# Kernel optimization log

Hardware: AMD Instinct MI355X
Metric: run time of the kernel (lower is better)

Reference implementation:

```python
import jax, jax.numpy as jnp
import numpy as np

N_AQI, N_MEO = 35, 18
N = N_AQI + N_MEO
F_OUT = 64
CTX = 60
D = F_OUT + CTX            # per-node feature dim inside pairwise concat
ALPHA = 0.2                # leakyrelu negative slope
B = 4096
IN_AQI, IN_MEO = 16, 16
NEG = -1e12


def _xavier(key, shape):
    fan_in, fan_out = shape[0], shape[-1]
    gain = 1.414
    bound = gain * np.sqrt(6.0 / (fan_in + fan_out))
    return jax.random.uniform(key, shape, jnp.float32, -bound, bound)


def setup_inputs() -> dict:
    key = jax.random.key(0)
    ks = jax.random.split(key, 32)
    inp = {
        "aqi_inp": jax.random.normal(ks[0], (B, N_AQI, IN_AQI), jnp.float32),
        "meo_inp": jax.random.normal(ks[1], (B, N_MEO, IN_MEO), jnp.float32),
        "context_feat": jax.random.normal(ks[2], (N, CTX), jnp.float32),
        "adj_norm": jax.random.uniform(ks[3], (N, N), jnp.float32),
        # embedding tables (all 2-dim embeddings as in the module)
        "aqi_idE": jax.random.normal(ks[4], (35, 2), jnp.float32),
        "aqi_monthE": jax.random.normal(ks[5], (13, 2), jnp.float32),
        "aqi_weekdayE": jax.random.normal(ks[6], (7, 2), jnp.float32),
        "aqi_hourE": jax.random.normal(ks[7], (24, 2), jnp.float32),
        "meo_windE": jax.random.normal(ks[8], (9, 2), jnp.float32),
        "meo_idE": jax.random.normal(ks[9], (18, 2), jnp.float32),
        "meo_monthE": jax.random.normal(ks[10], (13, 2), jnp.float32),
        "meo_weekdayE": jax.random.normal(ks[11], (7, 2), jnp.float32),
        "meo_hourE": jax.random.normal(ks[12], (24, 2), jnp.float32),
        # projection weights
        "W_xa": _xavier(ks[13], (IN_AQI, F_OUT)),
        "W_xm": _xavier(ks[14], (IN_MEO, F_OUT)),
        "W_ua": _xavier(ks[15], (IN_AQI + 8, F_OUT)),
        "W_um": _xavier(ks[16], (IN_MEO + 10, F_OUT)),
        # attention vectors: 2*F_OUT + 121 = 2*D + 1
        "a_aa": _xavier(ks[17], (2 * F_OUT + 121, 1)),
        "a_am": _xavier(ks[18], (2 * F_OUT + 121, 1)),
        "a_ma": _xavier(ks[19], (2 * F_OUT + 121, 1)),
        "a_mm": _xavier(ks[20], (2 * F_OUT + 121, 1)),
        # integer inputs
        "aqi_ex": jax.random.randint(ks[21], (B, N_AQI, 4), 0, 7, jnp.int32),
        "meo_ex": jax.random.randint(ks[22], (B, N_MEO, 5), 0, 7, jnp.int32),
        "adj": jax.random.randint(ks[23], (N, N), 0, 2, jnp.int32),
    }
    return inp


def _block(hf_src, hf_dst, an_block, a):
    # e[b,i,j] = leakyrelu(hf_src[b,i].a_src + hf_dst[b,j].a_dst + an[i,j]*a_last)
    d = hf_src.shape[-1]
    s = hf_src @ a[:d, 0]                        # [B, Ns]
    t = hf_dst @ a[d:2 * d, 0]                   # [B, Nd]
    e = s[:, :, None] + t[:, None, :] + an_block * a[2 * d, 0]
    return jax.nn.leaky_relu(e, ALPHA)


def reference(aqi_inp, meo_inp, context_feat, adj_norm,
              aqi_idE, aqi_monthE, aqi_weekdayE, aqi_hourE,
              meo_windE, meo_idE, meo_monthE, meo_weekdayE, meo_hourE,
              W_xa, W_xm, W_ua, W_um, a_aa, a_am, a_ma, a_mm,
              aqi_ex, meo_ex, adj):
    # value projection (pre-embedding features)
    attri_aqi = aqi_inp @ W_xa                   # [B, 35, F]
    attri_meo = meo_inp @ W_xm                   # [B, 18, F]
    heter_attri = jnp.concatenate([attri_aqi, attri_meo], axis=1)  # [B, 53, F]

    # append external-feature embeddings
    aqi_full = jnp.concatenate([
        aqi_inp, aqi_idE[aqi_ex[:, :, 0]], aqi_monthE[aqi_ex[:, :, 1]],
        aqi_weekdayE[aqi_ex[:, :, 2]], aqi_hourE[aqi_ex[:, :, 3]]], axis=2)
    meo_full = jnp.concatenate([
        meo_inp, meo_windE[meo_ex[:, :, 0]], meo_idE[meo_ex[:, :, 1]],
        meo_monthE[meo_ex[:, :, 2]], meo_weekdayE[meo_ex[:, :, 3]],
        meo_hourE[meo_ex[:, :, 4]]], axis=2)

    heter_aqi = aqi_full @ W_ua                  # [B, 35, F]
    heter_meo = meo_full @ W_um                  # [B, 18, F]
    hf = jnp.concatenate([heter_aqi, heter_meo], axis=1)            # [B, 53, F]
    ctx = jnp.broadcast_to(context_feat[None], (hf.shape[0], N, CTX))
    hf = jnp.concatenate([hf, ctx], axis=2)      # [B, 53, D]

    # pairwise scores per heterogeneous sub-block (decomposed, no N*N*D tensor)
    hfa, hfm = hf[:, :N_AQI], hf[:, N_AQI:]
    e_aa = _block(hfa, hfa, adj_norm[:N_AQI, :N_AQI], a_aa)
    e_am = _block(hfa, hfm, adj_norm[:N_AQI, N_AQI:], a_am)
    e_ma = _block(hfm, hfa, adj_norm[N_AQI:, :N_AQI], a_ma)
    e_mm = _block(hfm, hfm, adj_norm[N_AQI:, N_AQI:], a_mm)
    e = jnp.concatenate([
        jnp.concatenate([e_aa, e_am], axis=2),
        jnp.concatenate([e_ma, e_mm], axis=2)], axis=1)             # [B, 53, 53]

    attention = jax.nn.softmax(jnp.where(adj[None] > 0, e, NEG), axis=2)
    heter_out = attention @ heter_attri          # [B, 53, F]
    return heter_out[:, :N_AQI, :], heter_out[:, N_AQI:, :]
```

## Files before the change

kernel.cpp:

```cpp
#include <hip/hip_runtime.h>

#define NAQ 35
#define NME 18
#define NN  53
#define FD  64
#define CTXD 60
#define WAVES 8

typedef unsigned int   u32;
typedef unsigned short u16;
typedef short s8v __attribute__((ext_vector_type(8)));
typedef float f4v __attribute__((ext_vector_type(4)));

#define WS_EB_F  1280
#define WS_FLAG  4672

__device__ __forceinline__ float ldf(const void* p, long i, bool bf) {
  if (bf) { u16 h = ((const u16*)p)[i]; return __uint_as_float(((u32)h) << 16); }
  return ((const float*)p)[i];
}
__device__ __forceinline__ u16 f2bf(float f) {
  u32 u = __float_as_uint(f);
  return (u16)((u + 0x7FFFu + ((u >> 16) & 1u)) >> 16);
}
__device__ __forceinline__ float bf2f(u16 h) {
  return __uint_as_float(((u32)h) << 16);
}
__device__ __forceinline__ u32 pk2(float a, float b) {
  return (u32)f2bf(a) | ((u32)f2bf(b) << 16);
}
__device__ __forceinline__ bool sniff_bf16(const void* ctx) {
  const u32* w = (const u32*)ctx;
  bool ok = true;
#pragma unroll
  for (int k = 0; k < 32; ++k) {
    u32 e = (w[k] >> 7) & 0xFFu;
    ok = ok && (e >= 96u && e <= 160u);
  }
  return ok;
}
__device__ __forceinline__ s8v ld_fragu(const u16* p) {
  union { float4 f; s8v s; } u;
  u.f = *(const float4*)(const void*)p;
  return u.s;
}
__device__ __forceinline__ s8v pack8f(float4 a, float4 b) {
  union { u32 u[4]; s8v s; } U;
  U.u[0] = pk2(a.x, a.y);
  U.u[1] = pk2(a.z, a.w);
  U.u[2] = pk2(b.x, b.y);
  U.u[3] = pk2(b.z, b.w);
  return U.s;
}
__device__ __forceinline__ s8v load_inp8(const void* p, long idx, bool bf) {
  if (bf) {
    union { uint4 u; s8v s; } U;
    U.u = *(const uint4*)((const u16*)p + idx);
    return U.s;
  }
  float4 f0 = *(const float4*)((const float*)p + idx);
  float4 f1 = *(const float4*)((const float*)p + idx + 4);
  return pack8f(f0, f1);
}
__device__ __forceinline__ void pack_hl(const float* e, s8v* hi, s8v* lo) {
  union { u32 u[4]; s8v s; } H, L;
#pragma unroll
  for (int w = 0; w < 4; ++w) {
    u16 h0 = f2bf(e[2*w]), h1 = f2bf(e[2*w+1]);
    float l0 = e[2*w] - bf2f(h0), l1 = e[2*w+1] - bf2f(h1);
    H.u[w] = (u32)h0 | ((u32)h1 << 16);
    L.u[w] = (u32)f2bf(l0) | ((u32)f2bf(l1) << 16);
  }
  *hi = H.s; *lo = L.s;
}
__device__ __forceinline__ void avsel(int tr,
    const void* a_aa, const void* a_am, const void* a_ma, const void* a_mm,
    const void** av, int* off) {
  switch (tr) {
    case 0: *av = a_aa; *off = 0;   break;
    case 1: *av = a_am; *off = 0;   break;
    case 2: *av = a_aa; *off = 124; break;
    case 3: *av = a_ma; *off = 124; break;
    case 4: *av = a_ma; *off = 0;   break;
    case 5: *av = a_mm; *off = 0;   break;
    case 6: *av = a_am; *off = 124; break;
    default:*av = a_mm; *off = 124; break;
  }
}

__global__ void prep_kernel(
    const void* __restrict__ ctx, const void* __restrict__ adjn,
    const void* __restrict__ Wxa, const void* __restrict__ Wxm,
    const void* __restrict__ Wua, const void* __restrict__ Wum,
    const void* __restrict__ a_aa, const void* __restrict__ a_am,
    const void* __restrict__ a_ma, const void* __restrict__ a_mm,
    const int* __restrict__ adj, float* __restrict__ ws)
{
  const bool bf = sniff_bf16(ctx);
  int tid = blockIdx.x * blockDim.x + threadIdx.x;
  if (tid == 0) ws[WS_FLAG] = bf ? 1.f : 0.f;
  if (tid < 2048) {
    int n = tid >> 5, kk = tid & 31;
    float v = (kk < 16) ? ldf(Wxa, kk * 64 + n, bf)
                        : ldf(Wxm, (kk - 16) * 64 + n, bf);
    ((u16*)ws)[tid] = f2bf(v);
    return;
  }
  if (tid < 2560) {
    int idx = tid - 2048;
    int half = idx >> 8, rem = idx & 255;
    int role = rem >> 6, k = rem & 63;
    float w = 0.f;
    const void* Wu = nullptr; int kk = -1, tr = 0;
    if (k < 16)      { Wu = Wua; kk = k;           tr = role;     }
    else if (k < 32) { Wu = Wum; kk = k - 16;      tr = 4 + role; }
    else if (k < 40) { Wu = Wua; kk = 16 + (k-32); tr = role;     }
    else if (k < 50) { Wu = Wum; kk = 16 + (k-40); tr = 4 + role; }
    if (kk >= 0) {
      const void* av; int off;
      avsel(tr, a_aa, a_am, a_ma, a_mm, &av, &off);
      float s = 0.f;
      for (int f = 0; f < 64; ++f) s += ldf(Wu, kk * 64 + f, bf) * ldf(av, off + f, bf);
      w = s;
    }
    u16 hi = f2bf(w);
    u16 val = hi;
    if (half) { float lo = w - bf2f(hi); val = f2bf(lo); }
    ((u16*)ws)[2048 + idx] = val;
    return;
  }
  if (tid < 5952) {
    int e = tid - 2560;
    int r = e >> 6, j = e & 63;
    float v = 1e30f;
    if (j < NN && adj[r * NN + j] > 0) {
      const void* aq = (r < NAQ) ? ((j < NAQ) ? a_aa : a_am)
                                 : ((j < NAQ) ? a_ma : a_mm);
      float s = ldf(adjn, r * NN + j, bf) * ldf(aq, 248, bf);
      for (int c = 0; c < CTXD; ++c) {
        s += ldf(ctx, r * CTXD + c, bf) * ldf(aq, 64 + c, bf);
        s += ldf(ctx, j * CTXD + c, bf) * ldf(aq, 188 + c, bf);
      }
      v = s;
    }
    ws[WS_EB_F + e] = v;
  }
}

__global__ __launch_bounds__(512, 4) void hga_main(
    const void* __restrict__ aqi_inp, const void* __restrict__ meo_inp,
    const void* __restrict__ ctx,
    const void* __restrict__ aqi_idE, const void* __restrict__ aqi_monthE,
    const void* __restrict__ aqi_weekdayE, const void* __restrict__ aqi_hourE,
    const void* __restrict__ meo_windE, const void* __restrict__ meo_idE,
    const void* __restrict__ meo_monthE, const void* __restrict__ meo_weekdayE,
    const void* __restrict__ meo_hourE,
    const int* __restrict__ aqi_ex, const int* __restrict__ meo_ex,
    const float* __restrict__ ws, void* __restrict__ out, int B)
{
  __shared__ __align__(16) u16  sWtA[64 * 40];
  __shared__ __align__(16) u16  sWtPhi[16 * 72];
  __shared__ __align__(16) u16  sWtPlo[16 * 72];
  __shared__ __align__(16) float sEB[64 * 68];
  __shared__ __align__(16) float sSVW[WAVES * 256];

  const int t = threadIdx.x;
  const bool bf = (ws[WS_FLAG] != 0.f);
  const int wv = t >> 6, lane = t & 63;
  const int mm = lane & 15, q4 = lane >> 4;
  const int b = blockIdx.x * WAVES + wv;
  const bool valid = (b < B);

  s8v av0[4], a1h[4], a1l[4];
  const s8v zero8 = {0, 0, 0, 0, 0, 0, 0, 0};
#pragma unroll
  for (int i = 0; i < 4; ++i) { av0[i] = zero8; a1h[i] = zero8; a1l[i] = zero8; }
  if (valid) {
#pragma unroll
    for (int i = 0; i < 4; ++i) {
      const int r = 16 * i + mm;
      s8v v0 = zero8, vh = zero8, vl = zero8;
      if (r < NN) {
        if (r < NAQ) {
          if (q4 < 2) v0 = load_inp8(aqi_inp, ((long)b * NAQ + r) * 16 + q4 * 8, bf);
          if (q4 == 0) {
            const int4 ix = *(const int4*)(aqi_ex + ((long)b * NAQ + r) * 4);
            float e[8];
            e[0] = ldf(aqi_idE,      ix.x * 2, bf);  e[1] = ldf(aqi_idE,      ix.x * 2 + 1, bf);
            e[2] = ldf(aqi_monthE,   ix.y * 2, bf);  e[3] = ldf(aqi_monthE,   ix.y * 2 + 1, bf);
            e[4] = ldf(aqi_weekdayE, ix.z * 2, bf);  e[5] = ldf(aqi_weekdayE, ix.z * 2 + 1, bf);
            e[6] = ldf(aqi_hourE,    ix.w * 2, bf);  e[7] = ldf(aqi_hourE,    ix.w * 2 + 1, bf);
            pack_hl(e, &vh, &vl);
          }
        } else {
          const int ri = r - NAQ;
          if (q4 >= 2) v0 = load_inp8(meo_inp, ((long)b * NME + ri) * 16 + (q4 - 2) * 8, bf);
          if (q4 == 1) {
            const int* ix = meo_ex + ((long)b * NME + ri) * 5;
            float e[8];
            e[0] = ldf(meo_windE,    ix[0] * 2, bf); e[1] = ldf(meo_windE,    ix[0] * 2 + 1, bf);
            e[2] = ldf(meo_idE,      ix[1] * 2, bf); e[3] = ldf(meo_idE,      ix[1] * 2 + 1, bf);
            e[4] = ldf(meo_monthE,   ix[2] * 2, bf); e[5] = ldf(meo_monthE,   ix[2] * 2 + 1, bf);
            e[6] = ldf(meo_weekdayE, ix[3] * 2, bf); e[7] = ldf(meo_weekdayE, ix[3] * 2 + 1, bf);
            pack_hl(e, &vh, &vl);
          } else if (q4 == 2) {
            int i4 = meo_ex[((long)b * NME + ri) * 5 + 4];
            float e[8] = {0.f, 0.f, 0.f, 0.f, 0.f, 0.f, 0.f, 0.f};
            e[0] = ldf(meo_hourE, i4 * 2, bf);  e[1] = ldf(meo_hourE, i4 * 2 + 1, bf);
            pack_hl(e, &vh, &vl);
          }
        }
      }
      av0[i] = v0; a1h[i] = vh; a1l[i] = vl;
    }
  }

  for (int u = t; u < 256; u += 512) {
    int row = u >> 2, c = u & 3;
    *(uint4*)(sWtA + row * 40 + c * 8) = ((const uint4*)ws)[u];
  }
  for (int u = t; u < 256; u += 512) {
    int half = u >> 7, u2 = u & 127;
    int row = u2 >> 3, c = u2 & 7;
    uint4 v = make_uint4(0, 0, 0, 0);
    if (row < 4) v = ((const uint4*)ws)[256 + half * 32 + row * 8 + c];
    u16* dst = half ? sWtPlo : sWtPhi;
    *(uint4*)(dst + row * 72 + c * 8) = v;
  }
  for (int u = t; u < 1024; u += 512) {
    int r = u >> 4, f = u & 15;
    float4 v4 = make_float4(1e30f, 1e30f, 1e30f, 1e30f);
    if (r < NN) v4 = *(const float4*)(ws + WS_EB_F + r * 64 + f * 4);
    *(float4*)(sEB + r * 68 + f * 4) = v4;
  }
  __syncthreads();
  if (!valid) return;

  {
    s8v bh0 = ld_fragu(sWtPhi + mm * 72 + q4 * 8);
    s8v bh1 = ld_fragu(sWtPhi + mm * 72 + (4 + q4) * 8);
    s8v bl0 = ld_fragu(sWtPlo + mm * 72 + q4 * 8);
    s8v bl1 = ld_fragu(sWtPlo + mm * 72 + (4 + q4) * 8);
    f4v pacc[4];
#pragma unroll
    for (int i = 0; i < 4; ++i) {
      f4v a = {0.f, 0.f, 0.f, 0.f};
      a = __builtin_amdgcn_mfma_f32_16x16x32_bf16(av0[i], bh0, a, 0, 0, 0);
      a = __builtin_amdgcn_mfma_f32_16x16x32_bf16(av0[i], bl0, a, 0, 0, 0);
      a = __builtin_amdgcn_mfma_f32_16x16x32_bf16(a1h[i], bh1, a, 0, 0, 0);
      a = __builtin_amdgcn_mfma_f32_16x16x32_bf16(a1h[i], bl1, a, 0, 0, 0);
      if (!bf)
        a = __builtin_amdgcn_mfma_f32_16x16x32_bf16(a1l[i], bh1, a, 0, 0, 0);
      pacc[i] = a;
    }
    if (mm < 4) {
      float* wbase = sSVW + wv * 256 + ((mm >= 2) ? 128 : 0) + (mm & 1);
#pragma unroll
      for (int i = 0; i < 4; ++i)
#pragma unroll
        for (int reg = 0; reg < 4; ++reg) {
          int row = 16 * i + q4 * 4 + reg;
          wbase[row * 2] = pacc[i][reg];
        }
    }
  }
  asm volatile("s_waitcnt lgkmcnt(0)" ::: "memory");
  __builtin_amdgcn_sched_barrier(0);

  const float* sv = sSVW + wv * 256;
  u32 paw[4][8];
#pragma unroll
  for (int i = 0; i < 4; ++i) {
    const int r = 16 * i + mm;
    const bool rA = (r < NAQ);
    const int tsel = rA ? 0 : 1;
    float2 sp = *(const float2*)(sv + r * 2);
    const float* ebr = sEB + r * 68;
    float4 ea  = *(const float4*)(ebr + q4 * 8);
    float4 eb_ = *(const float4*)(ebr + q4 * 8 + 4);
    float4 ec  = *(const float4*)(ebr + 32 + q4 * 8);
    float4 ed  = *(const float4*)(ebr + 32 + q4 * 8 + 4);
    float ebv[16] = {ea.x, ea.y, ea.z, ea.w, eb_.x, eb_.y, eb_.z, eb_.w,
                     ec.x, ec.y, ec.z, ec.w, ed.x, ed.y, ed.z, ed.w};
    float v[16];
    float m = -3.0e38f;
#pragma unroll
    for (int c = 0; c < 16; ++c) {
      const int j = (c < 8) ? (q4 * 8 + c) : (32 + q4 * 8 + (c - 8));
      float s = (j < NAQ) ? sp.x : sp.y;
      float tv = sv[128 + j * 2 + tsel];
      float x = s + tv + ebv[c];
      float lk = fmaxf(x, 0.2f * x);
      float val = (ebv[c] > 1e29f) ? -1.0e12f : lk;
      v[c] = val;
      m = fmaxf(m, val);
    }
    m = fmaxf(m, __shfl_xor(m, 16));
    m = fmaxf(m, __shfl_xor(m, 32));
    float sum = 0.f;
#pragma unroll
    for (int c = 0; c < 16; ++c) { float p = __expf(v[c] - m); v[c] = p; sum += p; }
    sum += __shfl_xor(sum, 16);
    sum += __shfl_xor(sum, 32);
    const float rinv = 1.f / sum;
#pragma unroll
    for (int w = 0; w < 8; ++w) {
      const int c0 = (w >> 2) * 8 + (w & 3) * 2;
      paw[i][w] = pk2(v[c0] * rinv, v[c0 + 1] * rinv);
    }
  }

  const u32 baseA = (u32)b * (NAQ * 64u);
  const u32 baseM = (u32)B * (NAQ * 64u) + (u32)b * (NME * 64u);
  const int srcA = (2 * (q4 & 1)) * 16 + mm;
  const int srcB = srcA + 16;
  const bool hs = (q4 >= 2);
  __builtin_amdgcn_s_setprio(1);
#pragma unroll
  for (int nt = 0; nt < 4; ++nt) {
    s8v bw = ld_fragu(sWtA + (16 * nt + mm) * 40 + q4 * 8);
    f4v ag[4];
#pragma unroll
    for (int i = 0; i < 4; ++i) {
      f4v z = {0.f, 0.f, 0.f, 0.f};
      ag[i] = __builtin_amdgcn_mfma_f32_16x16x32_bf16(av0[i], bw, z, 0, 0, 0);
    }
    u32 p0[4], p1[4];
#pragma unroll
    for (int i = 0; i < 4; ++i) {
      p0[i] = pk2(ag[i][0], ag[i][1]);
      p1[i] = pk2(ag[i][2], ag[i][3]);
    }
    union { u32 u[4]; s8v s; } W0, W1;
    u32 x0, x1;
    x0 = (u32)__shfl((int)p0[0], srcA); x1 = (u32)__shfl((int)p0[1], srcA); W0.u[0] = hs ? x1 : x0;
    x0 = (u32)__shfl((int)p1[0], srcA); x1 = (u32)__shfl((int)p1[1], srcA); W0.u[1] = hs ? x1 : x0;
    x0 = (u32)__shfl((int)p0[0], srcB); x1 = (u32)__shfl((int)p0[1], srcB); W0.u[2] = hs ? x1 : x0;
    x0 = (u32)__shfl((int)p1[0], srcB); x1 = (u32)__shfl((int)p1[1], srcB); W0.u[3] = hs ? x1 : x0;
    x0 = (u32)__shfl((int)p0[2], srcA); x1 = (u32)__shfl((int)p0[3], srcA); W1.u[0] = hs ? x1 : x0;
    x0 = (u32)__shfl((int)p1[2], srcA); x1 = (u32)__shfl((int)p1[3], srcA); W1.u[1] = hs ? x1 : x0;
    x0 = (u32)__shfl((int)p0[2], srcB); x1 = (u32)__shfl((int)p0[3], srcB); W1.u[2] = hs ? x1 : x0;
    x0 = (u32)__shfl((int)p1[2], srcB); x1 = (u32)__shfl((int)p1[3], srcB); W1.u[3] = hs ? x1 : x0;
    s8v bt0 = W0.s, bt1 = W1.s;
#pragma unroll
    for (int i = 0; i < 4; ++i) {
      union { u32 u[4]; s8v s; } A0, A1;
      A0.u[0] = paw[i][0]; A0.u[1] = paw[i][1]; A0.u[2] = paw[i][2]; A0.u[3] = paw[i][3];
      A1.u[0] = paw[i][4]; A1.u[1] = paw[i][5]; A1.u[2] = paw[i][6]; A1.u[3] = paw[i][7];
      f4v acc = {0.f, 0.f, 0.f, 0.f};
      acc = __builtin_amdgcn_mfma_f32_16x16x32_bf16(bt0, A0.s, acc, 0, 0, 0);
      acc = __builtin_amdgcn_mfma_f32_16x16x32_bf16(bt1, A1.s, acc, 0, 0, 0);
      const int r = 16 * i + mm;
      if (r < NN) {
        u32 off = ((r < NAQ) ? (baseA + (u32)r * 64u)
                             : (baseM + (u32)(r - NAQ) * 64u))
                  + 16u * (u32)nt + (u32)(q4 * 4);
        if (bf) {
          uint2 pkv;
          pkv.x = pk2(acc[0], acc[1]);
          pkv.y = pk2(acc[2], acc[3]);
          *(uint2*)((u16*)out + off) = pkv;
        } else {
          union { f4v v; float4 f; } cv; cv.v = acc;
          *(float4*)((float*)out + off) = cv.f;
        }
      }
    }
  }
  __builtin_amdgcn_s_setprio(0);
}

extern "C" void kernel_launch(void* const* d_in, const int* in_sizes, int n_in,
                              void* d_out, int out_size, void* d_ws, size_t ws_size,
                              hipStream_t stream)
{
  const void* aqi_inp      = d_in[0];
  const void* meo_inp      = d_in[1];
  const void* ctx          = d_in[2];
  const void* adjn         = d_in[3];
  const void* aqi_idE      = d_in[4];
  const void* aqi_monthE   = d_in[5];
  const void* aqi_weekdayE = d_in[6];
  const void* aqi_hourE    = d_in[7];
  const void* meo_windE    = d_in[8];
  const void* meo_idE      = d_in[9];
  const void* meo_monthE   = d_in[10];
  const void* meo_weekdayE = d_in[11];
  const void* meo_hourE    = d_in[12];
  const void* Wxa          = d_in[13];
  const void* Wxm          = d_in[14];
  const void* Wua          = d_in[15];
  const void* Wum          = d_in[16];
  const void* a_aa         = d_in[17];
  const void* a_am         = d_in[18];
  const void* a_ma         = d_in[19];
  const void* a_mm         = d_in[20];
  const int*  aqi_ex       = (const int*)d_in[21];
  const int*  meo_ex       = (const int*)d_in[22];
  float* ws = (float*)d_ws;
  const int B = in_sizes[0] / (NAQ * 16);

  hipLaunchKernelGGL(prep_kernel, dim3((5952 + 255) / 256), dim3(256), 0, stream,
                     ctx, adjn, Wxa, Wxm, Wua, Wum, a_aa, a_am, a_ma, a_mm,
                     (const int*)d_in[23], ws);
  hipLaunchKernelGGL(hga_main, dim3((B + WAVES - 1) / WAVES), dim3(512), 0, stream,
                     aqi_inp, meo_inp, ctx, aqi_idE, aqi_monthE, aqi_weekdayE, aqi_hourE,
                     meo_windE, meo_idE, meo_monthE, meo_weekdayE, meo_hourE,
                     aqi_ex, meo_ex, ws, d_out, B);
}
```

Before: 152.1 us.

## Process two batch elements per wave to amortize shared-memory setup

Each wave now handles two batch elements, so every block covers twice as many elements and the grid is halved. The staging of weights and the edge-bias table into shared memory is amortized over more work. The second element's fragment loads are issued after the barrier so they can overlap with computation setup. The cost is higher register pressure, a relaxed launch bound, and fewer resident waves, which could reduce latency hiding.

```diff
diff --git a/kernel.cpp b/kernel.cpp
--- a/kernel.cpp
+++ b/kernel.cpp
@@ -6,6 +6,7 @@
 #define FD  64
 #define CTXD 60
 #define WAVES 8
+#define PERW 2
 
 typedef unsigned int   u32;
 typedef unsigned short u16;
@@ -147,95 +148,65 @@
   }
 }
 
-__global__ __launch_bounds__(512, 4) void hga_main(
-    const void* __restrict__ aqi_inp, const void* __restrict__ meo_inp,
-    const void* __restrict__ ctx,
-    const void* __restrict__ aqi_idE, const void* __restrict__ aqi_monthE,
-    const void* __restrict__ aqi_weekdayE, const void* __restrict__ aqi_hourE,
-    const void* __restrict__ meo_windE, const void* __restrict__ meo_idE,
-    const void* __restrict__ meo_monthE, const void* __restrict__ meo_weekdayE,
-    const void* __restrict__ meo_hourE,
-    const int* __restrict__ aqi_ex, const int* __restrict__ meo_ex,
-    const float* __restrict__ ws, void* __restrict__ out, int B)
+__device__ __forceinline__ void load_frags(
+    int b, bool valid, bool bf, int mm, int q4,
+    const void* aqi_inp, const void* meo_inp,
+    const void* aqi_idE, const void* aqi_monthE,
+    const void* aqi_weekdayE, const void* aqi_hourE,
+    const void* meo_windE, const void* meo_idE,
+    const void* meo_monthE, const void* meo_weekdayE, const void* meo_hourE,
+    const int* aqi_ex, const int* meo_ex,
+    s8v av0[4], s8v a1h[4], s8v a1l[4])
 {
-  __shared__ __align__(16) u16  sWtA[64 * 40];
-  __shared__ __align__(16) u16  sWtPhi[16 * 72];
-  __shared__ __align__(16) u16  sWtPlo[16 * 72];
-  __shared__ __align__(16) float sEB[64 * 68];
-  __shared__ __align__(16) float sSVW[WAVES * 256];
-
-  const int t = threadIdx.x;
-  const bool bf = (ws[WS_FLAG] != 0.f);
-  const int wv = t >> 6, lane = t & 63;
-  const int mm = lane & 15, q4 = lane >> 4;
-  const int b = blockIdx.x * WAVES + wv;
-  const bool valid = (b < B);
-
-  s8v av0[4], a1h[4], a1l[4];
   const s8v zero8 = {0, 0, 0, 0, 0, 0, 0, 0};
 #pragma unroll
   for (int i = 0; i < 4; ++i) { av0[i] = zero8; a1h[i] = zero8; a1l[i] = zero8; }
-  if (valid) {
-#pragma unroll
-    for (int i = 0; i < 4; ++i) {
-      const int r = 16 * i + mm;
-      s8v v0 = zero8, vh = zero8, vl = zero8;
-      if (r < NN) {
-        if (r < NAQ) {
-          if (q4 < 2) v0 = load_inp8(aqi_inp, ((long)b * NAQ + r) * 16 + q4 * 8, bf);
-          if (q4 == 0) {
-            const int4 ix = *(const int4*)(aqi_ex + ((long)b * NAQ + r) * 4);
-            float e[8];
-            e[0] = ldf(aqi_idE,      ix.x * 2, bf);  e[1] = ldf(aqi_idE,      ix.x * 2 + 1, bf);
-            e[2] = ldf(aqi_monthE,   ix.y * 2, bf);  e[3] = ldf(aqi_monthE,   ix.y * 2 + 1, bf);
-            e[4] = ldf(aqi_weekdayE, ix.z * 2, bf);  e[5] = ldf(aqi_weekdayE, ix.z * 2 + 1, bf);
-            e[6] = ldf(aqi_hourE,    ix.w * 2, bf);  e[7] = ldf(aqi_hourE,    ix.w * 2 + 1, bf);
-            pack_hl(e, &vh, &vl);
-          }
-        } else {
-          const int ri = r - NAQ;
-          if (q4 >= 2) v0 = load_inp8(meo_inp, ((long)b * NME + ri) * 16 + (q4 - 2) * 8, bf);
-          if (q4 == 1) {
-            const int* ix = meo_ex + ((long)b * NME + ri) * 5;
-            float e[8];
-            e[0] = ldf(meo_windE,    ix[0] * 2, bf); e[1] = ldf(meo_windE,    ix[0] * 2 + 1, bf);
-            e[2] = ldf(meo_idE,      ix[1] * 2, bf); e[3] = ldf(meo_idE,      ix[1] * 2 + 1, bf);
-            e[4] = ldf(meo_monthE,   ix[2] * 2, bf); e[5] = ldf(meo_monthE,   ix[2] * 2 + 1, bf);
-            e[6] = ldf(meo_weekdayE, ix[3] * 2, bf); e[7] = ldf(meo_weekdayE, ix[3] * 2 + 1, bf);
-            pack_hl(e, &vh, &vl);
-          } else if (q4 == 2) {
-            int i4 = meo_ex[((long)b * NME + ri) * 5 + 4];
-            float e[8] = {0.f, 0.f, 0.f, 0.f, 0.f, 0.f, 0.f, 0.f};
-            e[0] = ldf(meo_hourE, i4 * 2, bf);  e[1] = ldf(meo_hourE, i4 * 2 + 1, bf);
-            pack_hl(e, &vh, &vl);
-          }
+  if (!valid) return;
+#pragma unroll
+  for (int i = 0; i < 4; ++i) {
+    const int r = 16 * i + mm;
+    s8v v0 = zero8, vh = zero8, vl = zero8;
+    if (r < NN) {
+      if (r < NAQ) {
+        if (q4 < 2) v0 = load_inp8(aqi_inp, ((long)b * NAQ + r) * 16 + q4 * 8, bf);
+        if (q4 == 0) {
+          const int4 ix = *(const int4*)(aqi_ex + ((long)b * NAQ + r) * 4);
+          float e[8];
+          e[0] = ldf(aqi_idE,      ix.x * 2, bf);  e[1] = ldf(aqi_idE,      ix.x * 2 + 1, bf);
+          e[2] = ldf(aqi_monthE,   ix.y * 2, bf);  e[3] = ldf(aqi_monthE,   ix.y * 2 + 1, bf);
+          e[4] = ldf(aqi_weekdayE, ix.z * 2, bf);  e[5] = ldf(aqi_weekdayE, ix.z * 2 + 1, bf);
+          e[6] = ldf(aqi_hourE,    ix.w * 2, bf);  e[7] = ldf(aqi_hourE,    ix.w * 2 + 1, bf);
+          pack_hl(e, &vh, &vl);
+        }
+      } else {
+        const int ri = r - NAQ;
+        if (q4 >= 2) v0 = load_inp8(meo_inp, ((long)b * NME + ri) * 16 + (q4 - 2) * 8, bf);
+        if (q4 == 1) {
+          const int* ix = meo_ex + ((long)b * NME + ri) * 5;
+          float e[8];
+          e[0] = ldf(meo_windE,    ix[0] * 2, bf); e[1] = ldf(meo_windE,    ix[0] * 2 + 1, bf);
+          e[2] = ldf(meo_idE,      ix[1] * 2, bf); e[3] = ldf(meo_idE,      ix[1] * 2 + 1, bf);
+          e[4] = ldf(meo_monthE,   ix[2] * 2, bf); e[5] = ldf(meo_monthE,   ix[2] * 2 + 1, bf);
+          e[6] = ldf(meo_weekdayE, ix[3] * 2, bf); e[7] = ldf(meo_weekdayE, ix[3] * 2 + 1, bf);
+          pack_hl(e, &vh, &vl);
+        } else if (q4 == 2) {
+          int i4 = meo_ex[((long)b * NME + ri) * 5 + 4];
+          float e[8] = {0.f, 0.f, 0.f, 0.f, 0.f, 0.f, 0.f, 0.f};
+          e[0] = ldf(meo_hourE, i4 * 2, bf);  e[1] = ldf(meo_hourE, i4 * 2 + 1, bf);
+          pack_hl(e, &vh, &vl);
         }
       }
-      av0[i] = v0; a1h[i] = vh; a1l[i] = vl;
-    }
-  }
-
-  for (int u = t; u < 256; u += 512) {
-    int row = u >> 2, c = u & 3;
-    *(uint4*)(sWtA + row * 40 + c * 8) = ((const uint4*)ws)[u];
-  }
-  for (int u = t; u < 256; u += 512) {
-    int half = u >> 7, u2 = u & 127;
-    int row = u2 >> 3, c = u2 & 7;
-    uint4 v = make_uint4(0, 0, 0, 0);
-    if (row < 4) v = ((const uint4*)ws)[256 + half * 32 + row * 8 + c];
-    u16* dst = half ? sWtPlo : sWtPhi;
-    *(uint4*)(dst + row * 72 + c * 8) = v;
-  }
-  for (int u = t; u < 1024; u += 512) {
-    int r = u >> 4, f = u & 15;
-    float4 v4 = make_float4(1e30f, 1e30f, 1e30f, 1e30f);
-    if (r < NN) v4 = *(const float4*)(ws + WS_EB_F + r * 64 + f * 4);
-    *(float4*)(sEB + r * 68 + f * 4) = v4;
-  }
-  __syncthreads();
-  if (!valid) return;
-
+    }
+    av0[i] = v0; a1h[i] = vh; a1l[i] = vl;
+  }
+}
+
+__device__ __forceinline__ void process_elem(
+    int b, bool bf, int B, int mm, int q4, int wv,
+    const s8v av0[4], const s8v a1h[4], const s8v a1l[4],
+    const u16* sWtA, const u16* sWtPhi, const u16* sWtPlo,
+    const float* sEB, float* sSVW, void* out)
+{
   {
     s8v bh0 = ld_fragu(sWtPhi + mm * 72 + q4 * 8);
     s8v bh1 = ld_fragu(sWtPhi + mm * 72 + (4 + q4) * 8);
@@ -368,6 +339,71 @@
     }
   }
   __builtin_amdgcn_s_setprio(0);
+}
+
+__global__ __launch_bounds__(512, 2) void hga_main(
+    const void* __restrict__ aqi_inp, const void* __restrict__ meo_inp,
+    const void* __restrict__ ctx,
+    const void* __restrict__ aqi_idE, const void* __restrict__ aqi_monthE,
+    const void* __restrict__ aqi_weekdayE, const void* __restrict__ aqi_hourE,
+    const void* __restrict__ meo_windE, const void* __restrict__ meo_idE,
+    const void* __restrict__ meo_monthE, const void* __restrict__ meo_weekdayE,
+    const void* __restrict__ meo_hourE,
+    const int* __restrict__ aqi_ex, const int* __restrict__ meo_ex,
+    const float* __restrict__ ws, void* __restrict__ out, int B)
+{
+  __shared__ __align__(16) u16  sWtA[64 * 40];
+  __shared__ __align__(16) u16  sWtPhi[16 * 72];
+  __shared__ __align__(16) u16  sWtPlo[16 * 72];
+  __shared__ __align__(16) float sEB[64 * 68];
+  __shared__ __align__(16) float sSVW[WAVES * 256];
+
+  const int t = threadIdx.x;
+  const bool bf = (ws[WS_FLAG] != 0.f);
+  const int wv = t >> 6, lane = t & 63;
+  const int mm = lane & 15, q4 = lane >> 4;
+  const int b0 = blockIdx.x * (WAVES * PERW) + wv * PERW;
+  const int b1 = b0 + 1;
+  const bool valid0 = (b0 < B), valid1 = (b1 < B);
+
+  s8v av0a[4], a1ha[4], a1la[4];
+  load_frags(b0, valid0, bf, mm, q4, aqi_inp, meo_inp,
+             aqi_idE, aqi_monthE, aqi_weekdayE, aqi_hourE,
+             meo_windE, meo_idE, meo_monthE, meo_weekdayE, meo_hourE,
+             aqi_ex, meo_ex, av0a, a1ha, a1la);
+
+  for (int u = t; u < 256; u += 512) {
+    int row = u >> 2, c = u & 3;
+    *(uint4*)(sWtA + row * 40 + c * 8) = ((const uint4*)ws)[u];
+  }
+  for (int u = t; u < 256; u += 512) {
+    int half = u >> 7, u2 = u & 127;
+    int row = u2 >> 3, c = u2 & 7;
+    uint4 v = make_uint4(0, 0, 0, 0);
+    if (row < 4) v = ((const uint4*)ws)[256 + half * 32 + row * 8 + c];
+    u16* dst = half ? sWtPlo : sWtPhi;
+    *(uint4*)(dst + row * 72 + c * 8) = v;
+  }
+  for (int u = t; u < 1024; u += 512) {
+    int r = u >> 4, f = u & 15;
+    float4 v4 = make_float4(1e30f, 1e30f, 1e30f, 1e30f);
+    if (r < NN) v4 = *(const float4*)(ws + WS_EB_F + r * 64 + f * 4);
+    *(float4*)(sEB + r * 68 + f * 4) = v4;
+  }
+  __syncthreads();
+
+  s8v av0b[4], a1hb[4], a1lb[4];
+  load_frags(b1, valid1, bf, mm, q4, aqi_inp, meo_inp,
+             aqi_idE, aqi_monthE, aqi_weekdayE, aqi_hourE,
+             meo_windE, meo_idE, meo_monthE, meo_weekdayE, meo_hourE,
+             aqi_ex, meo_ex, av0b, a1hb, a1lb);
+
+  if (valid0)
+    process_elem(b0, bf, B, mm, q4, wv, av0a, a1ha, a1la,
+                 sWtA, sWtPhi, sWtPlo, sEB, sSVW, out);
+  if (valid1)
+    process_elem(b1, bf, B, mm, q4, wv, av0b, a1hb, a1lb,
+                 sWtA, sWtPhi, sWtPlo, sEB, sSVW, out);
 }
 
 extern "C" void kernel_launch(void* const* d_in, const int* in_sizes, int n_in,
@@ -403,7 +439,9 @@
   hipLaunchKernelGGL(prep_kernel, dim3((5952 + 255) / 256), dim3(256), 0, stream,
                      ctx, adjn, Wxa, Wxm, Wua, Wum, a_aa, a_am, a_ma, a_mm,
                      (const int*)d_in[23], ws);
-  hipLaunchKernelGGL(hga_main, dim3((B + WAVES - 1) / WAVES), dim3(512), 0, stream,
+  const int elems_per_block = WAVES * PERW;
+  hipLaunchKernelGGL(hga_main, dim3((B + elems_per_block - 1) / elems_per_block),
+                     dim3(512), 0, stream,
                      aqi_inp, meo_inp, ctx, aqi_idE, aqi_monthE, aqi_weekdayE, aqi_hourE,
                      meo_windE, meo_idE, meo_monthE, meo_weekdayE, meo_hourE,
                      aqi_ex, meo_ex, ws, d_out, B);
```

Result: slower. 158.3 us (+4.0%).

## Read precomputed weights and edge biases directly from global memory instead of LDS

Applied to the files above, without the earlier changes.

Drops the per-block staging of the weight fragments and the edge-bias table into shared memory, along with the block-wide barrier. Each wave now loads its MFMA B-fragments and edge-bias rows straight from the workspace, relying on the cache. The prep kernel pre-scales scores by log2(e) so the softmax can use exp2f, and it pads the edge-bias table to 64 rows so out-of-range reads see the masked sentinel. This cuts LDS use and the sync, which may raise occupancy, at the cost of more global and cache traffic per wave.

```diff
diff --git a/kernel.cpp b/kernel.cpp
--- a/kernel.cpp
+++ b/kernel.cpp
@@ -13,7 +13,8 @@
 typedef float f4v __attribute__((ext_vector_type(4)));
 
 #define WS_EB_F  1280
-#define WS_FLAG  4672
+#define WS_FLAG  5376
+#define LOG2E    1.44269504f
 
 __device__ __forceinline__ float ldf(const void* p, long i, bool bf) {
   if (bf) { u16 h = ((const u16*)p)[i]; return __uint_as_float(((u32)h) << 16); }
@@ -121,7 +122,7 @@
       avsel(tr, a_aa, a_am, a_ma, a_mm, &av, &off);
       float s = 0.f;
       for (int f = 0; f < 64; ++f) s += ldf(Wu, kk * 64 + f, bf) * ldf(av, off + f, bf);
-      w = s;
+      w = s * LOG2E;
     }
     u16 hi = f2bf(w);
     u16 val = hi;
@@ -129,11 +130,11 @@
     ((u16*)ws)[2048 + idx] = val;
     return;
   }
-  if (tid < 5952) {
+  if (tid < 6656) {
     int e = tid - 2560;
     int r = e >> 6, j = e & 63;
     float v = 1e30f;
-    if (j < NN && adj[r * NN + j] > 0) {
+    if (r < NN && j < NN && adj[r * NN + j] > 0) {
       const void* aq = (r < NAQ) ? ((j < NAQ) ? a_aa : a_am)
                                  : ((j < NAQ) ? a_ma : a_mm);
       float s = ldf(adjn, r * NN + j, bf) * ldf(aq, 248, bf);
@@ -141,7 +142,7 @@
         s += ldf(ctx, r * CTXD + c, bf) * ldf(aq, 64 + c, bf);
         s += ldf(ctx, j * CTXD + c, bf) * ldf(aq, 188 + c, bf);
       }
-      v = s;
+      v = s * LOG2E;
     }
     ws[WS_EB_F + e] = v;
   }
@@ -158,10 +159,6 @@
     const int* __restrict__ aqi_ex, const int* __restrict__ meo_ex,
     const float* __restrict__ ws, void* __restrict__ out, int B)
 {
-  __shared__ __align__(16) u16  sWtA[64 * 40];
-  __shared__ __align__(16) u16  sWtPhi[16 * 72];
-  __shared__ __align__(16) u16  sWtPlo[16 * 72];
-  __shared__ __align__(16) float sEB[64 * 68];
   __shared__ __align__(16) float sSVW[WAVES * 256];
 
   const int t = threadIdx.x;
@@ -169,78 +166,57 @@
   const int wv = t >> 6, lane = t & 63;
   const int mm = lane & 15, q4 = lane >> 4;
   const int b = blockIdx.x * WAVES + wv;
-  const bool valid = (b < B);
+  if (b >= B) return;
 
   s8v av0[4], a1h[4], a1l[4];
   const s8v zero8 = {0, 0, 0, 0, 0, 0, 0, 0};
 #pragma unroll
-  for (int i = 0; i < 4; ++i) { av0[i] = zero8; a1h[i] = zero8; a1l[i] = zero8; }
-  if (valid) {
-#pragma unroll
-    for (int i = 0; i < 4; ++i) {
-      const int r = 16 * i + mm;
-      s8v v0 = zero8, vh = zero8, vl = zero8;
-      if (r < NN) {
-        if (r < NAQ) {
-          if (q4 < 2) v0 = load_inp8(aqi_inp, ((long)b * NAQ + r) * 16 + q4 * 8, bf);
-          if (q4 == 0) {
-            const int4 ix = *(const int4*)(aqi_ex + ((long)b * NAQ + r) * 4);
-            float e[8];
-            e[0] = ldf(aqi_idE,      ix.x * 2, bf);  e[1] = ldf(aqi_idE,      ix.x * 2 + 1, bf);
-            e[2] = ldf(aqi_monthE,   ix.y * 2, bf);  e[3] = ldf(aqi_monthE,   ix.y * 2 + 1, bf);
-            e[4] = ldf(aqi_weekdayE, ix.z * 2, bf);  e[5] = ldf(aqi_weekdayE, ix.z * 2 + 1, bf);
-            e[6] = ldf(aqi_hourE,    ix.w * 2, bf);  e[7] = ldf(aqi_hourE,    ix.w * 2 + 1, bf);
-            pack_hl(e, &vh, &vl);
-          }
-        } else {
-          const int ri = r - NAQ;
-          if (q4 >= 2) v0 = load_inp8(meo_inp, ((long)b * NME + ri) * 16 + (q4 - 2) * 8, bf);
-          if (q4 == 1) {
-            const int* ix = meo_ex + ((long)b * NME + ri) * 5;
-            float e[8];
-            e[0] = ldf(meo_windE,    ix[0] * 2, bf); e[1] = ldf(meo_windE,    ix[0] * 2 + 1, bf);
-            e[2] = ldf(meo_idE,      ix[1] * 2, bf); e[3] = ldf(meo_idE,      ix[1] * 2 + 1, bf);
-            e[4] = ldf(meo_monthE,   ix[2] * 2, bf); e[5] = ldf(meo_monthE,   ix[2] * 2 + 1, bf);
-            e[6] = ldf(meo_weekdayE, ix[3] * 2, bf); e[7] = ldf(meo_weekdayE, ix[3] * 2 + 1, bf);
-            pack_hl(e, &vh, &vl);
-          } else if (q4 == 2) {
-            int i4 = meo_ex[((long)b * NME + ri) * 5 + 4];
-            float e[8] = {0.f, 0.f, 0.f, 0.f, 0.f, 0.f, 0.f, 0.f};
-            e[0] = ldf(meo_hourE, i4 * 2, bf);  e[1] = ldf(meo_hourE, i4 * 2 + 1, bf);
-            pack_hl(e, &vh, &vl);
-          }
+  for (int i = 0; i < 4; ++i) {
+    const int r = 16 * i + mm;
+    s8v v0 = zero8, vh = zero8, vl = zero8;
+    if (r < NN) {
+      if (r < NAQ) {
+        if (q4 < 2) v0 = load_inp8(aqi_inp, ((long)b * NAQ + r) * 16 + q4 * 8, bf);
+        if (q4 == 0) {
+          const int4 ix = *(const int4*)(aqi_ex + ((long)b * NAQ + r) * 4);
+          float e[8];
+          e[0] = ldf(aqi_idE,      ix.x * 2, bf);  e[1] = ldf(aqi_idE,      ix.x * 2 + 1, bf);
+          e[2] = ldf(aqi_monthE,   ix.y * 2, bf);  e[3] = ldf(aqi_monthE,   ix.y * 2 + 1, bf);
+          e[4] = ldf(aqi_weekdayE, ix.z * 2, bf);  e[5] = ldf(aqi_weekdayE, ix.z * 2 + 1, bf);
+          e[6] = ldf(aqi_hourE,    ix.w * 2, bf);  e[7] = ldf(aqi_hourE,    ix.w * 2 + 1, bf);
+          pack_hl(e, &vh, &vl);
+        }
+      } else {
+        const int ri = r - NAQ;
+        if (q4 >= 2) v0 = load_inp8(meo_inp, ((long)b * NME + ri) * 16 + (q4 - 2) * 8, bf);
+        if (q4 == 1) {
+          const int* ix = meo_ex + ((long)b * NME + ri) * 5;
+          float e[8];
+          e[0] = ldf(meo_windE,    ix[0] * 2, bf); e[1] = ldf(meo_windE,    ix[0] * 2 + 1, bf);
+          e[2] = ldf(meo_idE,      ix[1] * 2, bf); e[3] = ldf(meo_idE,      ix[1] * 2 + 1, bf);
+          e[4] = ldf(meo_monthE,   ix[2] * 2, bf); e[5] = ldf(meo_monthE,   ix[2] * 2 + 1, bf);
+          e[6] = ldf(meo_weekdayE, ix[3] * 2, bf); e[7] = ldf(meo_weekdayE, ix[3] * 2 + 1, bf);
+          pack_hl(e, &vh, &vl);
+        } else if (q4 == 2) {
+          int i4 = meo_ex[((long)b * NME + ri) * 5 + 4];
+          float e[8] = {0.f, 0.f, 0.f, 0.f, 0.f, 0.f, 0.f, 0.f};
+          e[0] = ldf(meo_hourE, i4 * 2, bf);  e[1] = ldf(meo_hourE, i4 * 2 + 1, bf);
+          pack_hl(e, &vh, &vl);
         }
       }
-      av0[i] = v0; a1h[i] = vh; a1l[i] = vl;
-    }
-  }
-
-  for (int u = t; u < 256; u += 512) {
-    int row = u >> 2, c = u & 3;
-    *(uint4*)(sWtA + row * 40 + c * 8) = ((const uint4*)ws)[u];
-  }
-  for (int u = t; u < 256; u += 512) {
-    int half = u >> 7, u2 = u & 127;
-    int row = u2 >> 3, c = u2 & 7;
-    uint4 v = make_uint4(0, 0, 0, 0);
-    if (row < 4) v = ((const uint4*)ws)[256 + half * 32 + row * 8 + c];
-    u16* dst = half ? sWtPlo : sWtPhi;
-    *(uint4*)(dst + row * 72 + c * 8) = v;
-  }
-  for (int u = t; u < 1024; u += 512) {
-    int r = u >> 4, f = u & 15;
-    float4 v4 = make_float4(1e30f, 1e30f, 1e30f, 1e30f);
-    if (r < NN) v4 = *(const float4*)(ws + WS_EB_F + r * 64 + f * 4);
-    *(float4*)(sEB + r * 68 + f * 4) = v4;
-  }
-  __syncthreads();
-  if (!valid) return;
+    }
+    av0[i] = v0; a1h[i] = vh; a1l[i] = vl;
+  }
+
+  const u16* wsu  = (const u16*)ws;
+  const u16* wphi = wsu + 2048;
+  const u16* wplo = wsu + 2304;
 
   {
-    s8v bh0 = ld_fragu(sWtPhi + mm * 72 + q4 * 8);
-    s8v bh1 = ld_fragu(sWtPhi + mm * 72 + (4 + q4) * 8);
-    s8v bl0 = ld_fragu(sWtPlo + mm * 72 + q4 * 8);
-    s8v bl1 = ld_fragu(sWtPlo + mm * 72 + (4 + q4) * 8);
+    s8v bh0 = ld_fragu(wphi + mm * 64 + q4 * 8);
+    s8v bh1 = ld_fragu(wphi + mm * 64 + 32 + q4 * 8);
+    s8v bl0 = ld_fragu(wplo + mm * 64 + q4 * 8);
+    s8v bl1 = ld_fragu(wplo + mm * 64 + 32 + q4 * 8);
     f4v pacc[4];
 #pragma unroll
     for (int i = 0; i < 4; ++i) {
@@ -275,7 +251,7 @@
     const bool rA = (r < NAQ);
     const int tsel = rA ? 0 : 1;
     float2 sp = *(const float2*)(sv + r * 2);
-    const float* ebr = sEB + r * 68;
+    const float* ebr = ws + WS_EB_F + r * 64;
     float4 ea  = *(const float4*)(ebr + q4 * 8);
     float4 eb_ = *(const float4*)(ebr + q4 * 8 + 4);
     float4 ec  = *(const float4*)(ebr + 32 + q4 * 8);
@@ -299,7 +275,7 @@
     m = fmaxf(m, __shfl_xor(m, 32));
     float sum = 0.f;
 #pragma unroll
-    for (int c = 0; c < 16; ++c) { float p = __expf(v[c] - m); v[c] = p; sum += p; }
+    for (int c = 0; c < 16; ++c) { float p = exp2f(v[c] - m); v[c] = p; sum += p; }
     sum += __shfl_xor(sum, 16);
     sum += __shfl_xor(sum, 32);
     const float rinv = 1.f / sum;
@@ -318,7 +294,7 @@
   __builtin_amdgcn_s_setprio(1);
 #pragma unroll
   for (int nt = 0; nt < 4; ++nt) {
-    s8v bw = ld_fragu(sWtA + (16 * nt + mm) * 40 + q4 * 8);
+    s8v bw = ld_fragu(wsu + (16 * nt + mm) * 32 + q4 * 8);
     f4v ag[4];
 #pragma unroll
     for (int i = 0; i < 4; ++i) {
@@ -400,7 +376,7 @@
   float* ws = (float*)d_ws;
   const int B = in_sizes[0] / (NAQ * 16);
 
-  hipLaunchKernelGGL(prep_kernel, dim3((5952 + 255) / 256), dim3(256), 0, stream,
+  hipLaunchKernelGGL(prep_kernel, dim3((6656 + 255) / 256), dim3(256), 0, stream,
                      ctx, adjn, Wxa, Wxm, Wua, Wum, a_aa, a_am, a_ma, a_mm,
                      (const int*)d_in[23], ws);
   hipLaunchKernelGGL(hga_main, dim3((B + WAVES - 1) / WAVES), dim3(512), 0, stream,
```

New measurement: 159.6 us. +4.9%, slower.

## Stage embedding lookups cooperatively in LDS and fold log2e into scores

Applied to the files above, without the earlier changes.

Embedding gathers for each node are moved out of per-lane divergent loads, where only one quarter of the lanes did work. All threads in the block now do them cooperatively, one thread per node, and write the packed hi/lo bf16 pairs into a new shared buffer that the MFMA fragments read after the barrier. The attention score precomputation multiplies by log2(e) so the softmax can use exp2f instead of __expf. The max reduction becomes a tree. The change adds about 18 KB of LDS per block, which may reduce occupancy below the launch_bounds target. The scaled scores are only equivalent because LeakyReLU is positively homogeneous.

```diff
diff --git a/kernel.cpp b/kernel.cpp
--- a/kernel.cpp
+++ b/kernel.cpp
@@ -14,6 +14,7 @@
 
 #define WS_EB_F  1280
 #define WS_FLAG  4672
+#define LOG2E    1.44269504f
 
 __device__ __forceinline__ float ldf(const void* p, long i, bool bf) {
   if (bf) { u16 h = ((const u16*)p)[i]; return __uint_as_float(((u32)h) << 16); }
@@ -121,7 +122,7 @@
       avsel(tr, a_aa, a_am, a_ma, a_mm, &av, &off);
       float s = 0.f;
       for (int f = 0; f < 64; ++f) s += ldf(Wu, kk * 64 + f, bf) * ldf(av, off + f, bf);
-      w = s;
+      w = s * LOG2E;
     }
     u16 hi = f2bf(w);
     u16 val = hi;
@@ -141,7 +142,7 @@
         s += ldf(ctx, r * CTXD + c, bf) * ldf(aq, 64 + c, bf);
         s += ldf(ctx, j * CTXD + c, bf) * ldf(aq, 188 + c, bf);
       }
-      v = s;
+      v = s * LOG2E;
     }
     ws[WS_EB_F + e] = v;
   }
@@ -163,6 +164,7 @@
   __shared__ __align__(16) u16  sWtPlo[16 * 72];
   __shared__ __align__(16) float sEB[64 * 68];
   __shared__ __align__(16) float sSVW[WAVES * 256];
+  __shared__ __align__(16) u16  sEMB[WAVES * 1136];
 
   const int t = threadIdx.x;
   const bool bf = (ws[WS_FLAG] != 0.f);
@@ -171,47 +173,58 @@
   const int b = blockIdx.x * WAVES + wv;
   const bool valid = (b < B);
 
-  s8v av0[4], a1h[4], a1l[4];
+  s8v av0[4];
   const s8v zero8 = {0, 0, 0, 0, 0, 0, 0, 0};
 #pragma unroll
-  for (int i = 0; i < 4; ++i) { av0[i] = zero8; a1h[i] = zero8; a1l[i] = zero8; }
-  if (valid) {
-#pragma unroll
-    for (int i = 0; i < 4; ++i) {
-      const int r = 16 * i + mm;
-      s8v v0 = zero8, vh = zero8, vl = zero8;
-      if (r < NN) {
-        if (r < NAQ) {
-          if (q4 < 2) v0 = load_inp8(aqi_inp, ((long)b * NAQ + r) * 16 + q4 * 8, bf);
-          if (q4 == 0) {
-            const int4 ix = *(const int4*)(aqi_ex + ((long)b * NAQ + r) * 4);
-            float e[8];
-            e[0] = ldf(aqi_idE,      ix.x * 2, bf);  e[1] = ldf(aqi_idE,      ix.x * 2 + 1, bf);
-            e[2] = ldf(aqi_monthE,   ix.y * 2, bf);  e[3] = ldf(aqi_monthE,   ix.y * 2 + 1, bf);
-            e[4] = ldf(aqi_weekdayE, ix.z * 2, bf);  e[5] = ldf(aqi_weekdayE, ix.z * 2 + 1, bf);
-            e[6] = ldf(aqi_hourE,    ix.w * 2, bf);  e[7] = ldf(aqi_hourE,    ix.w * 2 + 1, bf);
-            pack_hl(e, &vh, &vl);
-          }
-        } else {
-          const int ri = r - NAQ;
-          if (q4 >= 2) v0 = load_inp8(meo_inp, ((long)b * NME + ri) * 16 + (q4 - 2) * 8, bf);
-          if (q4 == 1) {
-            const int* ix = meo_ex + ((long)b * NME + ri) * 5;
-            float e[8];
-            e[0] = ldf(meo_windE,    ix[0] * 2, bf); e[1] = ldf(meo_windE,    ix[0] * 2 + 1, bf);
-            e[2] = ldf(meo_idE,      ix[1] * 2, bf); e[3] = ldf(meo_idE,      ix[1] * 2 + 1, bf);
-            e[4] = ldf(meo_monthE,   ix[2] * 2, bf); e[5] = ldf(meo_monthE,   ix[2] * 2 + 1, bf);
-            e[6] = ldf(meo_weekdayE, ix[3] * 2, bf); e[7] = ldf(meo_weekdayE, ix[3] * 2 + 1, bf);
-            pack_hl(e, &vh, &vl);
-          } else if (q4 == 2) {
-            int i4 = meo_ex[((long)b * NME + ri) * 5 + 4];
-            float e[8] = {0.f, 0.f, 0.f, 0.f, 0.f, 0.f, 0.f, 0.f};
-            e[0] = ldf(meo_hourE, i4 * 2, bf);  e[1] = ldf(meo_hourE, i4 * 2 + 1, bf);
-            pack_hl(e, &vh, &vl);
-          }
-        }
+  for (int i = 0; i < 4; ++i) {
+    s8v v0 = zero8;
+    const int r = 16 * i + mm;
+    if (valid && r < NN) {
+      if (r < NAQ) {
+        if (q4 < 2) v0 = load_inp8(aqi_inp, ((long)b * NAQ + r) * 16 + q4 * 8, bf);
+      } else {
+        if (q4 >= 2) v0 = load_inp8(meo_inp, ((long)b * NME + (r - NAQ)) * 16 + (q4 - 2) * 8, bf);
       }
-      av0[i] = v0; a1h[i] = vh; a1l[i] = vl;
+    }
+    av0[i] = v0;
+  }
+
+  if (t < WAVES * NN) {
+    const int el = t / NN;
+    const int r  = t - el * NN;
+    const int bb = blockIdx.x * WAVES + el;
+    if (bb < B) {
+      u16* dst = sEMB + el * 1136;
+      union { s8v s; uint4 u; } H, L;
+      if (r < NAQ) {
+        const int4 ix = *(const int4*)(aqi_ex + ((long)bb * NAQ + r) * 4);
+        float e[8];
+        e[0] = ldf(aqi_idE,      ix.x * 2, bf);  e[1] = ldf(aqi_idE,      ix.x * 2 + 1, bf);
+        e[2] = ldf(aqi_monthE,   ix.y * 2, bf);  e[3] = ldf(aqi_monthE,   ix.y * 2 + 1, bf);
+        e[4] = ldf(aqi_weekdayE, ix.z * 2, bf);  e[5] = ldf(aqi_weekdayE, ix.z * 2 + 1, bf);
+        e[6] = ldf(aqi_hourE,    ix.w * 2, bf);  e[7] = ldf(aqi_hourE,    ix.w * 2 + 1, bf);
+        pack_hl(e, &H.s, &L.s);
+        *(uint4*)(dst + r * 16)     = H.u;
+        *(uint4*)(dst + r * 16 + 8) = L.u;
+      } else {
+        const int ri = r - NAQ;
+        const int* ix = meo_ex + ((long)bb * NME + ri) * 5;
+        float e[8];
+        e[0] = ldf(meo_windE,    ix[0] * 2, bf); e[1] = ldf(meo_windE,    ix[0] * 2 + 1, bf);
+        e[2] = ldf(meo_idE,      ix[1] * 2, bf); e[3] = ldf(meo_idE,      ix[1] * 2 + 1, bf);
+        e[4] = ldf(meo_monthE,   ix[2] * 2, bf); e[5] = ldf(meo_monthE,   ix[2] * 2 + 1, bf);
+        e[6] = ldf(meo_weekdayE, ix[3] * 2, bf); e[7] = ldf(meo_weekdayE, ix[3] * 2 + 1, bf);
+        pack_hl(e, &H.s, &L.s);
+        u16* d2 = dst + 560 + ri * 32;
+        *(uint4*)(d2)     = H.u;
+        *(uint4*)(d2 + 8) = L.u;
+        float e2[8] = {0.f, 0.f, 0.f, 0.f, 0.f, 0.f, 0.f, 0.f};
+        e2[0] = ldf(meo_hourE, ix[4] * 2, bf);
+        e2[1] = ldf(meo_hourE, ix[4] * 2 + 1, bf);
+        pack_hl(e2, &H.s, &L.s);
+        *(uint4*)(d2 + 16) = H.u;
+        *(uint4*)(d2 + 24) = L.u;
+      }
     }
   }
 
@@ -235,6 +248,23 @@
   }
   __syncthreads();
   if (!valid) return;
+
+  s8v a1h[4], a1l[4];
+  const u16* myemb = sEMB + wv * 1136;
+#pragma unroll
+  for (int i = 0; i < 4; ++i) {
+    a1h[i] = zero8; a1l[i] = zero8;
+    const int r = 16 * i + mm;
+    if (r < NN) {
+      if (r < NAQ) {
+        if (q4 == 0) { a1h[i] = ld_fragu(myemb + r * 16); a1l[i] = ld_fragu(myemb + r * 16 + 8); }
+      } else {
+        const int ri = r - NAQ;
+        if (q4 == 1)      { a1h[i] = ld_fragu(myemb + 560 + ri * 32);      a1l[i] = ld_fragu(myemb + 560 + ri * 32 + 8); }
+        else if (q4 == 2) { a1h[i] = ld_fragu(myemb + 560 + ri * 32 + 16); a1l[i] = ld_fragu(myemb + 560 + ri * 32 + 24); }
+      }
+    }
+  }
 
   {
     s8v bh0 = ld_fragu(sWtPhi + mm * 72 + q4 * 8);
@@ -283,7 +313,6 @@
     float ebv[16] = {ea.x, ea.y, ea.z, ea.w, eb_.x, eb_.y, eb_.z, eb_.w,
                      ec.x, ec.y, ec.z, ec.w, ed.x, ed.y, ed.z, ed.w};
     float v[16];
-    float m = -3.0e38f;
 #pragma unroll
     for (int c = 0; c < 16; ++c) {
       const int j = (c < 8) ? (q4 * 8 + c) : (32 + q4 * 8 + (c - 8));
@@ -291,15 +320,18 @@
       float tv = sv[128 + j * 2 + tsel];
       float x = s + tv + ebv[c];
       float lk = fmaxf(x, 0.2f * x);
-      float val = (ebv[c] > 1e29f) ? -1.0e12f : lk;
-      v[c] = val;
-      m = fmaxf(m, val);
-    }
+      v[c] = (ebv[c] > 1e29f) ? -1.0e12f : lk;
+    }
+    float t0 = fmaxf(fmaxf(v[0], v[1]),  fmaxf(v[2], v[3]));
+    float t1 = fmaxf(fmaxf(v[4], v[5]),  fmaxf(v[6], v[7]));
+    float t2 = fmaxf(fmaxf(v[8], v[9]),  fmaxf(v[10], v[11]));
+    float t3 = fmaxf(fmaxf(v[12], v[13]), fmaxf(v[14], v[15]));
+    float m = fmaxf(fmaxf(t0, t1), fmaxf(t2, t3));
     m = fmaxf(m, __shfl_xor(m, 16));
     m = fmaxf(m, __shfl_xor(m, 32));
     float sum = 0.f;
 #pragma unroll
-    for (int c = 0; c < 16; ++c) { float p = __expf(v[c] - m); v[c] = p; sum += p; }
+    for (int c = 0; c < 16; ++c) { float p = exp2f(v[c] - m); v[c] = p; sum += p; }
     sum += __shfl_xor(sum, 16);
     sum += __shfl_xor(sum, 32);
     const float rinv = 1.f / sum;
```

Measured after the change: 152.6 us. Within noise of the previous version (+0.3%).
